# Performance work log

Measured on AMD Instinct MI355X. Metric: run time of the kernel, lower is better.

The kernel has to match this reference:

```python
import jax, jax.numpy as jnp
import numpy as np

N_NODES = 50000
N_EDGES = 800000
IN_DIM = 256
HID_DIM = 256
BATCH = 1


def setup_inputs() -> dict:
    key = jax.random.key(0)
    k1, k2, k3, k4, k5, k6, k7 = jax.random.split(key, 7)
    x = jax.random.normal(k1, (BATCH, N_NODES, IN_DIM), dtype=jnp.float32)
    edge_index = jax.random.randint(k2, (2, N_EDGES), 0, N_NODES, dtype=jnp.int32)
    # GCNConv params (glorot-ish scale)
    W1 = jax.random.normal(k3, (IN_DIM, HID_DIM), dtype=jnp.float32) * (1.0 / np.sqrt(IN_DIM))
    b1 = jnp.zeros((HID_DIM,), dtype=jnp.float32)
    W2 = jax.random.normal(k4, (HID_DIM, IN_DIM), dtype=jnp.float32) * (1.0 / np.sqrt(HID_DIM))
    b2 = jnp.zeros((IN_DIM,), dtype=jnp.float32)
    return {"x": x, "edge_index": edge_index, "W1": W1, "b1": b1, "W2": W2, "b2": b2}


def _gcn_conv(x, src, dst, norm, W, b):
    # x: [B, N, F_in] -> [B, N, F_out]; src/dst/norm: [E + N] (self-loops appended)
    h = x @ W                                   # linear transform first (PyG GCNConv)
    msg = h[:, src, :] * norm[None, :, None]    # gather + degree normalization
    out = jnp.zeros(h.shape, h.dtype).at[:, dst, :].add(msg)  # scatter-add
    return out + b


def _gcn_norm(edge_index, num_nodes):
    # symmetric normalization with self-loops: 1/sqrt(deg_i * deg_j)
    loop = jnp.arange(num_nodes, dtype=edge_index.dtype)
    src = jnp.concatenate([edge_index[0], loop])
    dst = jnp.concatenate([edge_index[1], loop])
    deg = jax.ops.segment_sum(jnp.ones(dst.shape, jnp.float32), dst, num_segments=num_nodes)
    dinv = jnp.where(deg > 0, jax.lax.rsqrt(jnp.maximum(deg, 1.0)), 0.0)
    norm = dinv[src] * dinv[dst]
    return src, dst, norm


def reference(x, edge_index, W1, b1, W2, b2):
    src, dst, norm = _gcn_norm(edge_index, x.shape[1])
    h = jax.nn.relu(_gcn_conv(x, src, dst, norm, W1, b1))
    h = jax.nn.relu(_gcn_conv(h, src, dst, norm, W2, b2))
    return (x + h) * 0.5
```

## Files before the change

### kernel.cpp

```cpp
#include <hip/hip_runtime.h>
#include <stdint.h>

#define NN 50000
#define NPAD 50048
#define NE 800000
#define DIM 256
#define NCHUNK 8
#define ZROW NN
#define GLC 64

typedef __attribute__((ext_vector_type(8))) short short8;
typedef __attribute__((ext_vector_type(8))) unsigned short ushort8v;
typedef __attribute__((ext_vector_type(4))) float floatx4;
typedef __attribute__((ext_vector_type(2))) float float2v;
typedef __attribute__((ext_vector_type(4))) uint32_t uint4v;
typedef __attribute__((ext_vector_type(4))) int int4v;

__device__ __forceinline__ uint16_t f2bf(float f) {
  union { float f; uint32_t u; } v; v.f = f;
  uint32_t r = v.u + 0x7fffu + ((v.u >> 16) & 1u);
  return (uint16_t)(r >> 16);
}
__device__ __forceinline__ float bf2f(uint16_t h) {
  union { uint32_t u; float f; } v; v.u = ((uint32_t)h) << 16;
  return v.f;
}

__device__ __forceinline__ void pkacc(float2v& a, uint32_t u) {
  union { uint32_t u; float f; } lo, hi;
  lo.u = u << 16;
  hi.u = u & 0xffff0000u;
  float2v val;
  val[0] = lo.f;
  val[1] = hi.f;
  asm("v_pk_add_f32 %0, %1, %0" : "+v"(a) : "v"(val));
}

__device__ __forceinline__ void stage16(const uint16_t* gp, short* lbase, int lane) {
#if __has_builtin(__builtin_amdgcn_global_load_lds)
  __builtin_amdgcn_global_load_lds((__attribute__((address_space(1))) void*)gp,
                                   (__attribute__((address_space(3))) void*)lbase,
                                   16, 0, 0);
#else
  *(ushort8v*)((uint16_t*)lbase + lane * 8) = *(const ushort8v*)gp;
#endif
}

__global__ __launch_bounds__(256) void k_init(int* __restrict__ fill, uint16_t* __restrict__ g,
                                              uint16_t* __restrict__ gl,
                                              const float* __restrict__ W1,
                                              const float* __restrict__ W2,
                                              uint16_t* __restrict__ Wt1,
                                              uint16_t* __restrict__ Wt2) {
  __shared__ float t[32][33];
  if (blockIdx.x >= 1563) {
    int bid = blockIdx.x - 1563;
    const float* W = (bid < 64) ? W1 : W2;
    uint16_t* Wt = (bid < 64) ? Wt1 : Wt2;
    bid &= 63;
    int bx = bid & 7, by = bid >> 3;
    int tx = threadIdx.x & 31, ty = threadIdx.x >> 5;
#pragma unroll
    for (int q = 0; q < 4; ++q)
      t[ty + q * 8][tx] = W[(size_t)(by * 32 + ty + q * 8) * 256 + bx * 32 + tx];
    __syncthreads();
#pragma unroll
    for (int q = 0; q < 4; ++q)
      Wt[(size_t)(bx * 32 + ty + q * 8) * 256 + by * 32 + tx] = f2bf(t[tx][ty + q * 8]);
    return;
  }
  int i = blockIdx.x * 256 + threadIdx.x;
  if (i < 400000) {
    ushort8v z8 = {ZROW, ZROW, ZROW, ZROW, ZROW, ZROW, ZROW, ZROW};
    ((ushort8v*)gl)[i] = z8;
  }
  if (i < NPAD / 4) {
    int4v zz = {0, 0, 0, 0};
    ((int4v*)fill)[i] = zz;
  }
  if (blockIdx.x < NCHUNK) {
    uint32_t* q = (uint32_t*)(g + ((size_t)blockIdx.x * NPAD + NN) * 32);
    for (int k = threadIdx.x; k < 768; k += 256) q[k] = 0;
  }
}

__global__ __launch_bounds__(256) void k_fill(const int* __restrict__ src,
                                              const int* __restrict__ dst,
                                              int* __restrict__ fill,
                                              uint16_t* __restrict__ gl) {
  int e = blockIdx.x * 256 + threadIdx.x;
  if (e < NE) {
    int d = dst[e];
    int old = atomicAdd(&fill[d], 1);
    if (old < GLC - 1) gl[(size_t)d * GLC + old] = (uint16_t)src[e];
  }
}

#define BM 64
#define BK 32

template <int SPLIT>
__global__ __launch_bounds__(256) void k_gemm(const uint16_t* __restrict__ Ab,
                                              const float* __restrict__ Af,
                                              const uint16_t* __restrict__ Wt,
                                              const int* __restrict__ degp,
                                              uint16_t* __restrict__ gl,
                                              uint16_t* __restrict__ C, int M) {
  __shared__ short Ash[2][BM * BK];
  __shared__ short Asl[2][BM * BK];
  __shared__ short Bs[2][256 * BK];

  const int tid = threadIdx.x;
  const int wave = tid >> 6, lane = tid & 63;
  const int m16 = lane & 15, q = lane >> 4;
  const int rowBase = blockIdx.x * BM;
  const int rsub = lane >> 2;
  const int kch = (lane & 3) * 8;

  auto stageB = [&](int kc, int buf) {
#pragma unroll
    for (int p2 = 0; p2 < 4; ++p2) {
      int n = p2 * 64 + wave * 16 + rsub;
      stage16(Wt + (size_t)n * 256 + kc * 32 + kch, &Bs[buf][(p2 * 64 + wave * 16) * BK], lane);
    }
  };
  auto stageA = [&](int kc, int buf) {
    int r = rowBase + wave * 16 + rsub;
    stage16(Ab + ((size_t)kc * NPAD + r) * 32 + kch, &Ash[buf][(wave * 16) * BK], lane);
  };
  auto loadA = [&](int kc, float4& f0, float4& f1) {
    int r = rowBase + wave * 16 + rsub;
    int rs = r < NN ? r : NN - 1;
    const float* xp = Af + (size_t)rs * DIM + kc * 32 + kch;
    f0 = *(const float4*)xp;
    f1 = *(const float4*)(xp + 4);
  };
  auto writeA = [&](int buf, const float4& f0, const float4& f1) {
    float ff[8] = {f0.x, f0.y, f0.z, f0.w, f1.x, f1.y, f1.z, f1.w};
    short8 h8, l8;
#pragma unroll
    for (int u = 0; u < 8; ++u) {
      uint16_t hh = f2bf(ff[u]);
      h8[u] = (short)hh;
      l8[u] = (short)f2bf(ff[u] - bf2f(hh));
    }
    *(short8*)&Ash[buf][(wave * 16 + rsub) * BK + kch] = h8;
    *(short8*)&Asl[buf][(wave * 16 + rsub) * BK + kch] = l8;
  };

  floatx4 acc[4][4];
#pragma unroll
  for (int i = 0; i < 4; ++i)
#pragma unroll
    for (int j = 0; j < 4; ++j) acc[i][j] = (floatx4)(0.0f);

  if (SPLIT && tid < BM) {
    int d = rowBase + tid;
    if (d < NN) {
      int deg = degp[d];
      if (deg < GLC) gl[(size_t)d * GLC + deg] = (uint16_t)d;
    }
  }

  if (SPLIT) {
    float4 f0, f1;
    loadA(0, f0, f1);
    writeA(0, f0, f1);
  } else {
    stageA(0, 0);
  }
  stageB(0, 0);
  __syncthreads();

  for (int kc = 0; kc < 8; ++kc) {
    const int cur = kc & 1, nxt = cur ^ 1;
    float4 g0, g1;
    if (kc < 7) {
      if (SPLIT) loadA(kc + 1, g0, g1);
      else stageA(kc + 1, nxt);
      stageB(kc + 1, nxt);
    }

    short8 ah[4], al[4], b[4];
#pragma unroll
    for (int i = 0; i < 4; ++i) {
      int r = i * 16 + m16;
      ah[i] = *(const short8*)(&Ash[cur][r * BK + q * 8]);
      if (SPLIT) al[i] = *(const short8*)(&Asl[cur][r * BK + q * 8]);
    }
#pragma unroll
    for (int j = 0; j < 4; ++j) {
      int n = wave * 64 + j * 16 + m16;
      b[j] = *(const short8*)(&Bs[cur][n * BK + q * 8]);
    }
#pragma unroll
    for (int i = 0; i < 4; ++i)
#pragma unroll
      for (int j = 0; j < 4; ++j) {
        if (SPLIT)
          acc[i][j] = __builtin_amdgcn_mfma_f32_16x16x32_bf16(al[i], b[j], acc[i][j], 0, 0, 0);
        acc[i][j] = __builtin_amdgcn_mfma_f32_16x16x32_bf16(ah[i], b[j], acc[i][j], 0, 0, 0);
      }

    if (SPLIT && kc < 7) writeA(nxt, g0, g1);
    __syncthreads();
  }

#pragma unroll
  for (int i = 0; i < 4; ++i) {
#pragma unroll
    for (int reg = 0; reg < 4; ++reg) {
      int row = rowBase + i * 16 + q * 4 + reg;
      if (row < M) {
        float dv = rsqrtf((float)(degp[row] + 1));
#pragma unroll
        for (int j = 0; j < 4; ++j) {
          int col = wave * 64 + j * 16 + m16;
          C[((size_t)(col >> 5) * NPAD + row) * 32 + (col & 31)] = f2bf(acc[i][j][reg] * dv);
        }
      }
    }
  }
}

template <int FINAL>
__global__ __launch_bounds__(256) void k_agg(const uint16_t* __restrict__ gb,
                                             const uint16_t* __restrict__ gl,
                                             const int* __restrict__ degp,
                                             const float* __restrict__ bias,
                                             const float* __restrict__ x,
                                             uint16_t* __restrict__ outb,
                                             float* __restrict__ outf) {
  const int c = blockIdx.x & 7;
  const int dg = blockIdx.x >> 3;
  const int wave = threadIdx.x >> 6, lane = threadIdx.x & 63;
  const int dl = lane >> 4;
  const int s = (lane >> 2) & 3;
  const int fl = lane & 3;
  const int d = dg * 16 + wave * 4 + dl;
  const uint16_t* gp = gb + (size_t)c * NPAD * 32;
  const uint32_t coff = (uint32_t)fl * 8;
  const uint32_t* glr = (const uint32_t*)(gl + (size_t)d * GLC);

  uint32_t w0 = glr[s], w1 = glr[s + 4], w2 = glr[s + 8];

  auto gat = [&](uint32_t iu) -> uint4v {
    return *(const uint4v*)(gp + iu * 32u + coff);
  };

  uint4v v0 = gat(w0 & 0xffffu), v1 = gat(w0 >> 16);
  uint4v v2 = gat(w1 & 0xffffu), v3 = gat(w1 >> 16);
  uint4v v4 = gat(w2 & 0xffffu), v5 = gat(w2 >> 16);

  float2v acc2[4];
#pragma unroll
  for (int j = 0; j < 4; ++j) acc2[j] = (float2v)(0.0f);
#pragma unroll
  for (int j = 0; j < 4; ++j) {
    pkacc(acc2[j], v0[j]);
    pkacc(acc2[j], v1[j]);
    pkacc(acc2[j], v2[j]);
    pkacc(acc2[j], v3[j]);
    pkacc(acc2[j], v4[j]);
    pkacc(acc2[j], v5[j]);
  }

  int deg = degp[d];
  if (deg >= 24) {
    for (int k = 12 + s; 2 * k <= deg; k += 4) {
      uint32_t w = glr[k];
      uint4v va = gat(w & 0xffffu), vb = gat(w >> 16);
#pragma unroll
      for (int j = 0; j < 4; ++j) {
        pkacc(acc2[j], va[j]);
        pkacc(acc2[j], vb[j]);
      }
    }
  }

#pragma unroll
  for (int j = 0; j < 4; ++j) {
    acc2[j][0] += __shfl_xor(acc2[j][0], 4);
    acc2[j][1] += __shfl_xor(acc2[j][1], 4);
    acc2[j][0] += __shfl_xor(acc2[j][0], 8);
    acc2[j][1] += __shfl_xor(acc2[j][1], 8);
  }

  if (s == 0) {
    float dd = rsqrtf((float)(deg + 1));
    int feat = c * 32 + fl * 8;
    float4 b0 = *(const float4*)(bias + feat);
    float4 b1 = *(const float4*)(bias + feat + 4);
    float bb[8] = {b0.x, b0.y, b0.z, b0.w, b1.x, b1.y, b1.z, b1.w};
    float r[8];
#pragma unroll
    for (int j = 0; j < 4; ++j) {
      r[2 * j] = fmaxf(dd * acc2[j][0] + bb[2 * j], 0.f);
      r[2 * j + 1] = fmaxf(dd * acc2[j][1] + bb[2 * j + 1], 0.f);
    }
    if (FINAL) {
      float4 x0 = *(const float4*)(x + (size_t)d * DIM + feat);
      float4 x1 = *(const float4*)(x + (size_t)d * DIM + feat + 4);
      float xx[8] = {x0.x, x0.y, x0.z, x0.w, x1.x, x1.y, x1.z, x1.w};
      float4 o0, o1;
      o0.x = (xx[0] + r[0]) * 0.5f; o0.y = (xx[1] + r[1]) * 0.5f;
      o0.z = (xx[2] + r[2]) * 0.5f; o0.w = (xx[3] + r[3]) * 0.5f;
      o1.x = (xx[4] + r[4]) * 0.5f; o1.y = (xx[5] + r[5]) * 0.5f;
      o1.z = (xx[6] + r[6]) * 0.5f; o1.w = (xx[7] + r[7]) * 0.5f;
      *(float4*)(outf + (size_t)d * DIM + feat) = o0;
      *(float4*)(outf + (size_t)d * DIM + feat + 4) = o1;
    } else {
      ushort8v o;
#pragma unroll
      for (int t = 0; t < 8; ++t) o[t] = f2bf(r[t]);
      *(ushort8v*)(outb + ((size_t)c * NPAD + d) * 32 + fl * 8) = o;
    }
  }
}

extern "C" void kernel_launch(void* const* d_in, const int* in_sizes, int n_in,
                              void* d_out, int out_size, void* d_ws, size_t ws_size,
                              hipStream_t stream) {
  const float* x  = (const float*)d_in[0];
  const int*   ei = (const int*)d_in[1];
  const float* W1 = (const float*)d_in[2];
  const float* b1 = (const float*)d_in[3];
  const float* W2 = (const float*)d_in[4];
  const float* b2 = (const float*)d_in[5];
  float* out = (float*)d_out;

  int*      fill   = (int*)d_ws;
  uint16_t* gl     = (uint16_t*)(fill + NPAD);
  uint16_t* Wt1    = gl + (size_t)NN * GLC;
  uint16_t* Wt2    = Wt1 + 256 * 256;
  uint16_t* g      = Wt2 + 256 * 256;
  uint16_t* h1     = g + (size_t)NPAD * DIM;

  const int* esrc = ei;
  const int* edst = ei + NE;

  k_init<<<1691, 256, 0, stream>>>(fill, g, gl, W1, W2, Wt1, Wt2);
  k_fill<<<(NE + 255) / 256, 256, 0, stream>>>(esrc, edst, fill, gl);

  const int aggBlocks = NCHUNK * (NN / 16);
  const int gemmBlocks = NPAD / BM;
  k_gemm<1><<<gemmBlocks, 256, 0, stream>>>(nullptr, x, Wt1, fill, gl, g, NN);
  k_agg<0><<<aggBlocks, 256, 0, stream>>>(g, gl, fill, b1, nullptr, h1, nullptr);
  k_gemm<0><<<gemmBlocks, 256, 0, stream>>>(h1, nullptr, Wt2, fill, nullptr, g, NN);
  k_agg<1><<<aggBlocks, 256, 0, stream>>>(g, gl, fill, b2, x, nullptr, out);
}
```

Measured before the change: 290.6 us.

## Prefetch GEMM A tiles two stages ahead and vectorize edge fill loads

The GEMM now loads A data into registers two k-steps ahead and writes it to shared memory at the start of the next iteration. This replaces the direct staging for the bf16 path and the post-MFMA write for the split path, so global load latency overlaps with more MFMA work. Separately, the edge-list fill kernel reads src/dst as int4 vectors and processes four edges per thread. The changes cost extra registers and serialise four atomics per thread, which may reduce occupancy or atomic parallelism.

```diff
diff --git a/kernel.cpp b/kernel.cpp
--- a/kernel.cpp
+++ b/kernel.cpp
@@ -84,15 +84,20 @@
   }
 }
 
-__global__ __launch_bounds__(256) void k_fill(const int* __restrict__ src,
-                                              const int* __restrict__ dst,
+__global__ __launch_bounds__(256) void k_fill(const int4v* __restrict__ src4,
+                                              const int4v* __restrict__ dst4,
                                               int* __restrict__ fill,
                                               uint16_t* __restrict__ gl) {
-  int e = blockIdx.x * 256 + threadIdx.x;
-  if (e < NE) {
-    int d = dst[e];
-    int old = atomicAdd(&fill[d], 1);
-    if (old < GLC - 1) gl[(size_t)d * GLC + old] = (uint16_t)src[e];
+  int e4 = blockIdx.x * 256 + threadIdx.x;
+  if (e4 < NE / 4) {
+    int4v s = src4[e4];
+    int4v d = dst4[e4];
+#pragma unroll
+    for (int u = 0; u < 4; ++u) {
+      int dd = d[u];
+      int old = atomicAdd(&fill[dd], 1);
+      if (old < GLC - 1) gl[(size_t)dd * GLC + old] = (uint16_t)s[u];
+    }
   }
 }
 
@@ -117,6 +122,9 @@
   const int rsub = lane >> 2;
   const int kch = (lane & 3) * 8;
 
+  float4 f0, f1;
+  short8 a8;
+
   auto stageB = [&](int kc, int buf) {
 #pragma unroll
     for (int p2 = 0; p2 < 4; ++p2) {
@@ -124,28 +132,33 @@
       stage16(Wt + (size_t)n * 256 + kc * 32 + kch, &Bs[buf][(p2 * 64 + wave * 16) * BK], lane);
     }
   };
-  auto stageA = [&](int kc, int buf) {
-    int r = rowBase + wave * 16 + rsub;
-    stage16(Ab + ((size_t)kc * NPAD + r) * 32 + kch, &Ash[buf][(wave * 16) * BK], lane);
+  auto loadA = [&](int kc) {
+    if (SPLIT) {
+      int r = rowBase + wave * 16 + rsub;
+      int rs = r < NN ? r : NN - 1;
+      const float* xp = Af + (size_t)rs * DIM + kc * 32 + kch;
+      f0 = *(const float4*)xp;
+      f1 = *(const float4*)(xp + 4);
+    } else {
+      int r = rowBase + wave * 16 + rsub;
+      a8 = *(const short8*)(Ab + ((size_t)kc * NPAD + r) * 32 + kch);
+    }
   };
-  auto loadA = [&](int kc, float4& f0, float4& f1) {
-    int r = rowBase + wave * 16 + rsub;
-    int rs = r < NN ? r : NN - 1;
-    const float* xp = Af + (size_t)rs * DIM + kc * 32 + kch;
-    f0 = *(const float4*)xp;
-    f1 = *(const float4*)(xp + 4);
-  };
-  auto writeA = [&](int buf, const float4& f0, const float4& f1) {
-    float ff[8] = {f0.x, f0.y, f0.z, f0.w, f1.x, f1.y, f1.z, f1.w};
-    short8 h8, l8;
-#pragma unroll
-    for (int u = 0; u < 8; ++u) {
-      uint16_t hh = f2bf(ff[u]);
-      h8[u] = (short)hh;
-      l8[u] = (short)f2bf(ff[u] - bf2f(hh));
-    }
-    *(short8*)&Ash[buf][(wave * 16 + rsub) * BK + kch] = h8;
-    *(short8*)&Asl[buf][(wave * 16 + rsub) * BK + kch] = l8;
+  auto writeA = [&](int buf) {
+    if (SPLIT) {
+      float ff[8] = {f0.x, f0.y, f0.z, f0.w, f1.x, f1.y, f1.z, f1.w};
+      short8 h8, l8;
+#pragma unroll
+      for (int u = 0; u < 8; ++u) {
+        uint16_t hh = f2bf(ff[u]);
+        h8[u] = (short)hh;
+        l8[u] = (short)f2bf(ff[u] - bf2f(hh));
+      }
+      *(short8*)&Ash[buf][(wave * 16 + rsub) * BK + kch] = h8;
+      *(short8*)&Asl[buf][(wave * 16 + rsub) * BK + kch] = l8;
+    } else {
+      *(short8*)&Ash[buf][(wave * 16 + rsub) * BK + kch] = a8;
+    }
   };
 
   floatx4 acc[4][4];
@@ -162,24 +175,19 @@
     }
   }
 
-  if (SPLIT) {
-    float4 f0, f1;
-    loadA(0, f0, f1);
-    writeA(0, f0, f1);
-  } else {
-    stageA(0, 0);
-  }
+  loadA(0);
+  writeA(0);
   stageB(0, 0);
+  loadA(1);
   __syncthreads();
 
   for (int kc = 0; kc < 8; ++kc) {
     const int cur = kc & 1, nxt = cur ^ 1;
-    float4 g0, g1;
     if (kc < 7) {
-      if (SPLIT) loadA(kc + 1, g0, g1);
-      else stageA(kc + 1, nxt);
+      writeA(nxt);
       stageB(kc + 1, nxt);
     }
+    if (kc < 6) loadA(kc + 2);
 
     short8 ah[4], al[4], b[4];
 #pragma unroll
@@ -202,7 +210,6 @@
         acc[i][j] = __builtin_amdgcn_mfma_f32_16x16x32_bf16(ah[i], b[j], acc[i][j], 0, 0, 0);
       }
 
-    if (SPLIT && kc < 7) writeA(nxt, g0, g1);
     __syncthreads();
   }
 
@@ -336,11 +343,11 @@
   uint16_t* g      = Wt2 + 256 * 256;
   uint16_t* h1     = g + (size_t)NPAD * DIM;
 
-  const int* esrc = ei;
-  const int* edst = ei + NE;
+  const int4v* esrc4 = (const int4v*)ei;
+  const int4v* edst4 = (const int4v*)(ei + NE);
 
   k_init<<<1691, 256, 0, stream>>>(fill, g, gl, W1, W2, Wt1, Wt2);
-  k_fill<<<(NE + 255) / 256, 256, 0, stream>>>(esrc, edst, fill, gl);
+  k_fill<<<(NE / 4 + 255) / 256, 256, 0, stream>>>(esrc4, edst4, fill, gl);
 
   const int aggBlocks = NCHUNK * (NN / 16);
   const int gemmBlocks = NPAD / BM;
```

Measured after the change: 292.0 us. Within noise of the previous version (+0.5%).
